# Kernel tuning notes

Measured on AMD Instinct MI355X. Metric: run time of the kernel, lower is better.

## Reference

```python
import jax, jax.numpy as jnp
import numpy as np

B, N, S = 4, 16384, 16384
C1, C2 = 256, 256
D_MODEL, NHEAD, OUT_DIM = 256, 8, 256
HEAD_DIM = D_MODEL // NHEAD
EPS_ATTN = 1e-6


def _layernorm(x, g, b, eps=1e-5):
    mu = jnp.mean(x, axis=-1, keepdims=True)
    var = jnp.mean(jnp.square(x - mu), axis=-1, keepdims=True)
    return (x - mu) * jax.lax.rsqrt(var + eps) * g + b


def setup_inputs() -> dict:
    key = jax.random.key(0)
    ks = jax.random.split(key, 20)
    def w(k, shape, fan_in):
        return jax.random.normal(k, shape, jnp.float32) * (1.0 / np.sqrt(fan_in))
    return {
        "feat1": jax.random.normal(ks[0], (B, C1, N), jnp.float32),
        "xyz1": jax.random.normal(ks[1], (B, N, 3), jnp.float32),
        "feat2": jax.random.normal(ks[2], (B, C2, S), jnp.float32),
        "xyz2": jax.random.normal(ks[3], (B, S, 3), jnp.float32),
        # pos_mlp2: Linear(3, d_model) -> ReLU -> Linear(d_model, feat2_dim)
        "pos_w1": w(ks[4], (D_MODEL, 3), 3),
        "pos_b1": jnp.zeros((D_MODEL,), jnp.float32),
        "pos_w2": w(ks[5], (C2, D_MODEL), D_MODEL),
        "pos_b2": jnp.zeros((C2,), jnp.float32),
        "q_w": w(ks[6], (D_MODEL, C1), C1),
        "k_w": w(ks[7], (D_MODEL, C2), C2),
        "v_w": w(ks[8], (D_MODEL, C2), C2),
        "merge_w": w(ks[9], (D_MODEL, D_MODEL), D_MODEL),
        # mlp: Linear(C1 + d_model, 2*d_model) -> ReLU -> Linear(2*d_model, out_dim)
        "mlp_w1": w(ks[10], (2 * D_MODEL, C1 + D_MODEL), C1 + D_MODEL),
        "mlp_w2": w(ks[11], (OUT_DIM, 2 * D_MODEL), 2 * D_MODEL),
        "ln1_g": jnp.ones((D_MODEL,), jnp.float32),
        "ln1_b": jnp.zeros((D_MODEL,), jnp.float32),
        "ln2_g": jnp.ones((OUT_DIM,), jnp.float32),
        "ln2_b": jnp.zeros((OUT_DIM,), jnp.float32),
    }


def reference(feat1, xyz1, feat2, xyz2, pos_w1, pos_b1, pos_w2, pos_b2,
              q_w, k_w, v_w, merge_w, mlp_w1, mlp_w2,
              ln1_g, ln1_b, ln2_g, ln2_b):
    bs = feat1.shape[0]
    f1 = jnp.transpose(feat1, (0, 2, 1))  # [B, N, C1]
    f2 = jnp.transpose(feat2, (0, 2, 1))  # [B, S, C2]
    # positional MLP on xyz2 added to feat2
    pos = jax.nn.relu(xyz2 @ pos_w1.T + pos_b1) @ pos_w2.T + pos_b2
    f2p = f2 + pos
    q = (f1 @ q_w.T).reshape(bs, -1, NHEAD, HEAD_DIM)   # [B, N, H, D]
    k = (f2 @ k_w.T).reshape(bs, -1, NHEAD, HEAD_DIM)   # [B, S, H, D]
    v = (f2p @ v_w.T).reshape(bs, -1, NHEAD, HEAD_DIM)  # [B, S, H, D]
    # Linear attention (elu feature map)
    Q = jax.nn.elu(q) + 1.0
    K = jax.nn.elu(k) + 1.0
    v_len = v.shape[1]
    V = v / v_len
    KV = jnp.einsum('nshd,nshv->nhdv', K, V)                 # [B, H, D, D]
    Z = 1.0 / (jnp.einsum('nlhd,nhd->nlh', Q, K.sum(axis=1)) + EPS_ATTN)
    msg = jnp.einsum('nlhd,nhdv,nlh->nlhv', Q, KV, Z) * v_len  # [B, N, H, D]
    msg = msg.reshape(bs, -1, NHEAD * HEAD_DIM) @ merge_w.T
    msg = _layernorm(msg, ln1_g, ln1_b)
    msg = jnp.concatenate([f1, msg], axis=2)
    msg = jax.nn.relu(msg @ mlp_w1.T) @ mlp_w2.T
    msg = _layernorm(msg, ln2_g, ln2_b)
    return jnp.transpose(msg, (0, 2, 1))  # [B, out_dim, N]
```

## Files before the change

### kernel.cpp

```cpp
#include <hip/hip_runtime.h>


typedef float f32x4 __attribute__((ext_vector_type(4)));
typedef __bf16 bf16x8 __attribute__((ext_vector_type(8)));
typedef __bf16 bf16x4 __attribute__((ext_vector_type(4)));

#define MFMA16(a, b, c) __builtin_amdgcn_mfma_f32_16x16x32_bf16((a), (b), (c), 0, 0, 0)

__device__ __forceinline__ void gll16(const __bf16* g, __bf16* l) {
    __builtin_amdgcn_global_load_lds(
        (const __attribute__((address_space(1))) void*)g,
        (__attribute__((address_space(3))) void*)l, 16, 0, 0);
}

__global__ __launch_bounds__(256) void prep_weights_kernel(
    const float* __restrict__ s0, const float* __restrict__ s1,
    const float* __restrict__ s2, const float* __restrict__ s3,
    const float* __restrict__ s4, const float* __restrict__ s5,
    const float* __restrict__ s6,
    __bf16* __restrict__ d0, __bf16* __restrict__ d1, __bf16* __restrict__ d2,
    __bf16* __restrict__ d3, __bf16* __restrict__ d4, __bf16* __restrict__ d5,
    __bf16* __restrict__ d6, float* __restrict__ zbase)
{
    int idx = blockIdx.x * 256 + threadIdx.x;
    if (idx < 327680) {
        int seg = idx >> 16, off = idx & 65535;
        const float* s = (seg == 0) ? s0 : (seg == 1) ? s1 : (seg == 2) ? s2 : (seg == 3) ? s3 : s4;
        __bf16* d = (seg == 0) ? d0 : (seg == 1) ? d1 : (seg == 2) ? d2 : (seg == 3) ? d3 : d4;
        d[off] = (__bf16)s[off];
    } else if (idx < 589824) {
        int off = idx - 327680; d5[off] = (__bf16)s5[off];
    } else if (idx < 720896) {
        int off = idx - 589824; d6[off] = (__bf16)s6[off];
    } else if (idx < 754688) {
        zbase[idx - 720896] = 0.f;
    }
}

__global__ __launch_bounds__(256) void pos_hidden_kernel(
    const float* __restrict__ xyz2, const float* __restrict__ pw1,
    const float* __restrict__ pb1, __bf16* __restrict__ Hid)
{
    const int tid = threadIdx.x;
    size_t tok = (size_t)blockIdx.x * 8 + (tid >> 5);
    int c0 = (tid & 31) * 8;
    const float* xz = xyz2 + tok * 3;
    float x = xz[0], y = xz[1], z = xz[2];
    bf16x8 o;
    #pragma unroll
    for (int j = 0; j < 8; ++j) {
        const float* wr = pw1 + (size_t)(c0 + j) * 3;
        float h = fmaf(x, wr[0], fmaf(y, wr[1], fmaf(z, wr[2], pb1[c0 + j])));
        o[j] = (__bf16)fmaxf(h, 0.f);
    }
    *(bf16x8*)(Hid + tok * 256 + c0) = o;
}

__global__ __launch_bounds__(256) void transpose_cast_kernel(
    const float* __restrict__ In, __bf16* __restrict__ Outb)
{
    const int tid = threadIdx.x;
    const int t0 = blockIdx.x * 64, c0 = blockIdx.y * 64;
    const size_t b = blockIdx.z;
    __shared__ __bf16 tile[64 * 72];
    #pragma unroll
    for (int i = 0; i < 4; ++i) {
        int c = i * 16 + (tid >> 4);
        int t4 = (tid & 15) * 4;
        float4 v = *(const float4*)(In + (b * 256 + c0 + c) * 16384 + t0 + t4);
        tile[(t4 + 0) * 72 + c] = (__bf16)v.x;
        tile[(t4 + 1) * 72 + c] = (__bf16)v.y;
        tile[(t4 + 2) * 72 + c] = (__bf16)v.z;
        tile[(t4 + 3) * 72 + c] = (__bf16)v.w;
    }
    __syncthreads();
    #pragma unroll
    for (int i = 0; i < 2; ++i) {
        int chunk = tid + i * 256;
        int tr = chunk >> 3, c8 = (chunk & 7) * 8;
        bf16x8 v = *(const bf16x8*)(tile + tr * 72 + c8);
        *(bf16x8*)(Outb + (b * 16384 + t0 + tr) * 256 + c0 + c8) = v;
    }
}

enum { EPI_STORE = 0, EPI_ELU = 1, EPI_ADDB = 2, EPI_RELU = 3, EPI_ELU_KSUM = 4 };

template <int EPI, bool SPLIT>
__global__ __launch_bounds__(256, 4) void gemm_tok(
    const __bf16* __restrict__ Wg,
    const __bf16* __restrict__ A0,
    const __bf16* __restrict__ A1,
    __bf16* __restrict__ Outg,
    const float* __restrict__ bias,
    const __bf16* __restrict__ addg,
    float* __restrict__ KSg,
    int K, int Cout)
{
    const int tid = threadIdx.x, w = tid >> 6, l = tid & 63, lm = l & 15;
    const int gm0 = blockIdx.x * 128, gn0 = blockIdx.y * 128;
    const size_t b = blockIdx.z;
    const __bf16* A0b = A0 + b * 16384 * (size_t)256;
    const __bf16* A1b = SPLIT ? (A1 + b * 16384 * (size_t)256) : nullptr;
    __bf16* Outb = Outg + b * 16384 * (size_t)Cout;
    const __bf16* addb = (EPI == EPI_ADDB) ? (addg + b * 16384 * (size_t)256) : nullptr;

    __shared__ __bf16 Alds[2][128 * 32];
    __shared__ __bf16 Wlds[2][128 * 32];
    __shared__ float kred[16 * 64];

    f32x4 acc[4][4];
    #pragma unroll
    for (int i = 0; i < 4; ++i)
        #pragma unroll
        for (int j = 0; j < 4; ++j) acc[i][j] = (f32x4){0.f, 0.f, 0.f, 0.f};

    const int wm = (w >> 1) * 64, wn = (w & 1) * 64;
    const int srow = tid >> 2, scol = (tid & 3) * 8;
    const int koff = (l >> 4) * 8;
    const int wbase = w * 512;

    auto stage = [&](int buf, int ks) {
        const __bf16* As = A0b; int kk = ks;
        if (SPLIT && ks >= 256) { As = A1b; kk = ks - 256; }
        gll16(As + (size_t)(gm0 + srow) * 256 + kk + scol,      &Alds[buf][wbase]);
        gll16(As + (size_t)(gm0 + 64 + srow) * 256 + kk + scol, &Alds[buf][2048 + wbase]);
        gll16(Wg + (size_t)(gn0 + srow) * K + ks + scol,        &Wlds[buf][wbase]);
        gll16(Wg + (size_t)(gn0 + 64 + srow) * K + ks + scol,   &Wlds[buf][2048 + wbase]);
    };

    stage(0, 0);
    __syncthreads();
    int cur = 0;
    for (int ks = 0; ks < K; ks += 32) {
        if (ks + 32 < K) stage(cur ^ 1, ks + 32);
        bf16x8 af[4], wf[4];
        #pragma unroll
        for (int mf = 0; mf < 4; ++mf)
            af[mf] = *(const bf16x8*)&Alds[cur][(wm + mf * 16 + lm) * 32 + koff];
        #pragma unroll
        for (int nf = 0; nf < 4; ++nf)
            wf[nf] = *(const bf16x8*)&Wlds[cur][(wn + nf * 16 + lm) * 32 + koff];
        #pragma unroll
        for (int mf = 0; mf < 4; ++mf)
            #pragma unroll
            for (int nf = 0; nf < 4; ++nf)
                acc[mf][nf] = MFMA16(af[mf], wf[nf], acc[mf][nf]);
        __syncthreads();
        cur ^= 1;
    }

    const int r0 = (l >> 4) * 4;
    float kpart[4] = {0.f, 0.f, 0.f, 0.f};
    #pragma unroll
    for (int mf = 0; mf < 4; ++mf) {
        #pragma unroll
        for (int nf = 0; nf < 4; ++nf) {
            int tok = gm0 + wm + mf * 16 + r0;
            int ch  = gn0 + wn + nf * 16 + lm;
            #pragma unroll
            for (int r = 0; r < 4; ++r) {
                float v = acc[mf][nf][r];
                if (EPI == EPI_ELU || EPI == EPI_ELU_KSUM)
                    v = (v > 0.f) ? (v + 1.f) : __expf(v);
                if (EPI == EPI_RELU) v = fmaxf(v, 0.f);
                if (EPI == EPI_ADDB) v = v + bias[ch] + (float)addb[(size_t)(tok + r) * 256 + ch];
                if (EPI == EPI_ELU_KSUM) kpart[nf] += v;
                Outb[(size_t)(tok + r) * Cout + ch] = (__bf16)v;
            }
        }
    }
    if (EPI == EPI_ELU_KSUM) {
        #pragma unroll
        for (int nf = 0; nf < 4; ++nf)
            kred[(w * 4 + (l >> 4)) * 64 + nf * 16 + lm] = kpart[nf];
        __syncthreads();
        if (tid < 128) {
            int c = tid;
            int wsel = (c >= 64) ? 1 : 0;
            float s = 0.f;
            #pragma unroll
            for (int q = 0; q < 4; ++q)
                s += kred[((wsel * 4) + q) * 64 + (c & 63)]
                   + kred[(((wsel + 2) * 4) + q) * 64 + (c & 63)];
            atomicAdd(&KSg[b * 256 + gn0 + c], s);
        }
    }
}

__global__ __launch_bounds__(256) void kv_kernel(
    const __bf16* __restrict__ Kb, const __bf16* __restrict__ Vb,
    float* __restrict__ KVg)
{
    const int tid = threadIdx.x, w = tid >> 6, l = tid & 63, lm = l & 15;
    const int sc = blockIdx.x, h = blockIdx.y, b = blockIdx.z;
    __shared__ __bf16 kT[32 * 264];
    __shared__ __bf16 vT[32 * 264];
    __shared__ float red[4 * 32 * 32];

    f32x4 acc[2][2];
    #pragma unroll
    for (int i = 0; i < 2; ++i)
        #pragma unroll
        for (int j = 0; j < 2; ++j) acc[i][j] = (f32x4){0.f, 0.f, 0.f, 0.f};

    const int koff = (l >> 4) * 8, r0 = (l >> 4) * 4;
    const size_t rowbase = (size_t)b * 16384;
    bf16x4 kreg[8], vreg[8];
    auto loadsub = [&](int sub) {
        int s0 = sc * 1024 + sub * 256;
        #pragma unroll
        for (int pass = 0; pass < 8; ++pass) {
            int sl = pass * 32 + (tid >> 3);
            int c4 = (tid & 7) * 4;
            kreg[pass] = *(const bf16x4*)(Kb + (rowbase + s0 + sl) * 256 + h * 32 + c4);
            vreg[pass] = *(const bf16x4*)(Vb + (rowbase + s0 + sl) * 256 + h * 32 + c4);
        }
    };
    loadsub(0);
    for (int sub = 0; sub < 4; ++sub) {
        __syncthreads();
        #pragma unroll
        for (int pass = 0; pass < 8; ++pass) {
            int sl = pass * 32 + (tid >> 3);
            int c4 = (tid & 7) * 4;
            #pragma unroll
            for (int i = 0; i < 4; ++i) {
                kT[(c4 + i) * 264 + sl] = kreg[pass][i];
                vT[(c4 + i) * 264 + sl] = vreg[pass][i];
            }
        }
        __syncthreads();
        if (sub < 3) loadsub(sub + 1);
        #pragma unroll
        for (int kq = 0; kq < 2; ++kq) {
            int sb = w * 64 + kq * 32;
            bf16x8 af[2], bfr[2];
            #pragma unroll
            for (int mf = 0; mf < 2; ++mf)
                af[mf] = *(const bf16x8*)(kT + (mf * 16 + lm) * 264 + sb + koff);
            #pragma unroll
            for (int nf = 0; nf < 2; ++nf)
                bfr[nf] = *(const bf16x8*)(vT + (nf * 16 + lm) * 264 + sb + koff);
            #pragma unroll
            for (int mf = 0; mf < 2; ++mf)
                #pragma unroll
                for (int nf = 0; nf < 2; ++nf)
                    acc[mf][nf] = MFMA16(af[mf], bfr[nf], acc[mf][nf]);
        }
    }
    #pragma unroll
    for (int mf = 0; mf < 2; ++mf)
        #pragma unroll
        for (int nf = 0; nf < 2; ++nf)
            #pragma unroll
            for (int r = 0; r < 4; ++r) {
                int d = mf * 16 + r0 + r, e = nf * 16 + lm;
                red[w * 1024 + d * 32 + e] = acc[mf][nf][r];
            }
    __syncthreads();
    #pragma unroll
    for (int i = 0; i < 4; ++i) {
        int idx = tid + i * 256;
        float s = red[idx] + red[1024 + idx] + red[2048 + idx] + red[3072 + idx];
        atomicAdd(&KVg[((size_t)(b * 8 + h)) * 1024 + idx], s);
    }
}

__global__ __launch_bounds__(256) void attn_apply(
    const __bf16* __restrict__ Qb, const float* __restrict__ KVg,
    const float* __restrict__ KSg, __bf16* __restrict__ Msg)
{
    const int tid = threadIdx.x, w = tid >> 6, l = tid & 63, lm = l & 15;
    const int tok0 = blockIdx.x * 64;
    const size_t b = blockIdx.y;
    __shared__ __bf16 kvT[8 * 32 * 40];
    __shared__ float ks_lds[256], z_lds[64 * 8];

    const float* KVb = KVg + b * 8192;
    #pragma unroll
    for (int i = 0; i < 32; ++i) {
        int idx = tid + i * 256;
        int h = idx >> 10, d = (idx >> 5) & 31, e = idx & 31;
        kvT[(h * 32 + e) * 40 + d] = (__bf16)KVb[idx];
    }
    ks_lds[tid] = KSg[b * 256 + tid];
    __syncthreads();

    const __bf16* Qbase = Qb + (b * 16384 + tok0) * (size_t)256;
    #pragma unroll
    for (int i = 0; i < 2; ++i) {
        int p = tid + i * 256;
        int tok = p >> 3, h = p & 7;
        const __bf16* qr = Qbase + (size_t)tok * 256 + h * 32;
        float s = 0.f;
        #pragma unroll
        for (int j = 0; j < 4; ++j) {
            bf16x8 q8 = *(const bf16x8*)(qr + j * 8);
            #pragma unroll
            for (int t = 0; t < 8; ++t) s += (float)q8[t] * ks_lds[h * 32 + j * 8 + t];
        }
        z_lds[tok * 8 + h] = 1.f / (s + 1e-6f);
    }
    __syncthreads();

    const int koff = (l >> 4) * 8, r0 = (l >> 4) * 4;
    const f32x4 zero4 = (f32x4){0.f, 0.f, 0.f, 0.f};
    #pragma unroll
    for (int h = 0; h < 8; ++h) {
        bf16x8 af = *(const bf16x8*)(Qbase + (size_t)(w * 16 + lm) * 256 + h * 32 + koff);
        #pragma unroll
        for (int nf = 0; nf < 2; ++nf) {
            bf16x8 bv = *(const bf16x8*)(kvT + (h * 32 + nf * 16 + lm) * 40 + koff);
            f32x4 m = MFMA16(af, bv, zero4);
            #pragma unroll
            for (int r = 0; r < 4; ++r) {
                int tok = w * 16 + r0 + r;
                Msg[(b * 16384 + tok0 + tok) * (size_t)256 + h * 32 + nf * 16 + lm] =
                    (__bf16)(m[r] * z_lds[tok * 8 + h]);
            }
        }
    }
}

template <bool TRANS>
__global__ __launch_bounds__(256, 2) void gemm_ln(
    const __bf16* __restrict__ Ag,
    const __bf16* __restrict__ Wg,
    const float* __restrict__ gv, const float* __restrict__ bv,
    __bf16* __restrict__ OutB,
    float* __restrict__ OutF,
    int K)
{
    const int tid = threadIdx.x, w = tid >> 6, l = tid & 63, lm = l & 15;
    const int tok0 = blockIdx.x * 128;
    const size_t b = blockIdx.y;
    const size_t trow = b * 16384 + tok0;

    __shared__ __align__(16) char smem[49152];
    __bf16* AldsB = (__bf16*)smem;
    __bf16* WldsB = (__bf16*)(smem + 16384);
    __shared__ float red1[512], red2[512], mu_lds[128], rs_lds[128];
    __shared__ float g_lds[256], b_lds[256];
    g_lds[tid] = gv[tid];
    b_lds[tid] = bv[tid];

    f32x4 acc[8][4];
    #pragma unroll
    for (int i = 0; i < 8; ++i)
        #pragma unroll
        for (int j = 0; j < 4; ++j) acc[i][j] = (f32x4){0.f, 0.f, 0.f, 0.f};

    const int srow = tid >> 2, scol = (tid & 3) * 8;
    const int koff = (l >> 4) * 8, wn = w * 64, wbase = w * 512;

    auto stage = [&](int buf, int ks) {
        gll16(Ag + (trow + srow) * K + ks + scol,      AldsB + buf * 4096 + wbase);
        gll16(Ag + (trow + 64 + srow) * K + ks + scol, AldsB + buf * 4096 + 2048 + wbase);
        #pragma unroll
        for (int c = 0; c < 4; ++c)
            gll16(Wg + (size_t)(c * 64 + srow) * K + ks + scol,
                  WldsB + buf * 8192 + c * 2048 + wbase);
    };

    stage(0, 0);
    __syncthreads();
    int cur = 0;
    for (int ks = 0; ks < K; ks += 32) {
        if (ks + 32 < K) stage(cur ^ 1, ks + 32);
        bf16x8 af[8], wf[4];
        #pragma unroll
        for (int mf = 0; mf < 8; ++mf)
            af[mf] = *(const bf16x8*)(AldsB + cur * 4096 + (mf * 16 + lm) * 32 + koff);
        #pragma unroll
        for (int nf = 0; nf < 4; ++nf)
            wf[nf] = *(const bf16x8*)(WldsB + cur * 8192 + (wn + nf * 16 + lm) * 32 + koff);
        #pragma unroll
        for (int mf = 0; mf < 8; ++mf)
            #pragma unroll
            for (int nf = 0; nf < 4; ++nf)
                acc[mf][nf] = MFMA16(af[mf], wf[nf], acc[mf][nf]);
        __syncthreads();
        cur ^= 1;
    }

    const int r0 = (l >> 4) * 4;
    #pragma unroll
    for (int mf = 0; mf < 8; ++mf) {
        #pragma unroll
        for (int r = 0; r < 4; ++r) {
            float s1 = 0.f, s2 = 0.f;
            #pragma unroll
            for (int nf = 0; nf < 4; ++nf) { float v = acc[mf][nf][r]; s1 += v; s2 += v * v; }
            #pragma unroll
            for (int m = 1; m < 16; m <<= 1) { s1 += __shfl_xor(s1, m, 64); s2 += __shfl_xor(s2, m, 64); }
            if (lm == 0) {
                red1[w * 128 + mf * 16 + r0 + r] = s1;
                red2[w * 128 + mf * 16 + r0 + r] = s2;
            }
        }
    }
    __syncthreads();
    if (tid < 128) {
        float s1 = red1[tid] + red1[128 + tid] + red1[256 + tid] + red1[384 + tid];
        float s2 = red2[tid] + red2[128 + tid] + red2[256 + tid] + red2[384 + tid];
        float mu = s1 * (1.f / 256.f);
        mu_lds[tid] = mu;
        rs_lds[tid] = rsqrtf(s2 * (1.f / 256.f) - mu * mu + 1e-5f);
    }
    __syncthreads();

    if (TRANS) {
        float* wb = (float*)smem + w * 2112;
        #pragma unroll
        for (int nf = 0; nf < 4; ++nf) {
            __syncthreads();
            float gg = g_lds[wn + nf * 16 + lm], bb = b_lds[wn + nf * 16 + lm];
            #pragma unroll
            for (int mf = 0; mf < 8; ++mf) {
                int tl = mf * 16 + r0;
                f32x4 v;
                #pragma unroll
                for (int r = 0; r < 4; ++r)
                    v[r] = (acc[mf][nf][r] - mu_lds[tl + r]) * rs_lds[tl + r] * gg + bb;
                *(f32x4*)(wb + lm * 132 + tl) = v;
            }
            __syncthreads();
            #pragma unroll
            for (int t = 0; t < 8; ++t) {
                int row = t * 2 + (l >> 5);
                int col = (l & 31) * 4;
                f32x4 v = *(const f32x4*)(wb + row * 132 + col);
                *(f32x4*)(OutF + (b * 256 + wn + nf * 16 + row) * (size_t)16384 + tok0 + col) = v;
            }
        }
    } else {
        #pragma unroll
        for (int mf = 0; mf < 8; ++mf) {
            #pragma unroll
            for (int nf = 0; nf < 4; ++nf) {
                int ch = wn + nf * 16 + lm;
                #pragma unroll
                for (int r = 0; r < 4; ++r) {
                    int tl = mf * 16 + r0 + r;
                    float y = (acc[mf][nf][r] - mu_lds[tl]) * rs_lds[tl] * g_lds[ch] + b_lds[ch];
                    OutB[(trow + tl) * (size_t)256 + ch] = (__bf16)y;
                }
            }
        }
    }
}

extern "C" void kernel_launch(void* const* d_in, const int* in_sizes, int n_in,
                              void* d_out, int out_size, void* d_ws, size_t ws_size,
                              hipStream_t stream) {
    const float* feat1   = (const float*)d_in[0];
    const float* feat2   = (const float*)d_in[2];
    const float* xyz2    = (const float*)d_in[3];
    const float* pos_w1  = (const float*)d_in[4];
    const float* pos_b1  = (const float*)d_in[5];
    const float* pos_w2  = (const float*)d_in[6];
    const float* pos_b2  = (const float*)d_in[7];
    const float* q_w     = (const float*)d_in[8];
    const float* k_w     = (const float*)d_in[9];
    const float* v_w     = (const float*)d_in[10];
    const float* merge_w = (const float*)d_in[11];
    const float* mlp_w1  = (const float*)d_in[12];
    const float* mlp_w2  = (const float*)d_in[13];
    const float* ln1_g   = (const float*)d_in[14];
    const float* ln1_b   = (const float*)d_in[15];
    const float* ln2_g   = (const float*)d_in[16];
    const float* ln2_b   = (const float*)d_in[17];
    float* outp = (float*)d_out;

    char* ws = (char*)d_ws;
    size_t off = 0;
    auto alloc = [&](size_t bytes) { char* p = ws + off; off += (bytes + 255) & ~(size_t)255; return p; };
    const size_t ACT = (size_t)4 * 16384 * 256 * 2;
    __bf16* WQ  = (__bf16*)alloc(65536 * 2);
    __bf16* WK  = (__bf16*)alloc(65536 * 2);
    __bf16* WV  = (__bf16*)alloc(65536 * 2);
    __bf16* WM  = (__bf16*)alloc(65536 * 2);
    __bf16* WP2 = (__bf16*)alloc(65536 * 2);
    __bf16* W1  = (__bf16*)alloc(262144 * 2);
    __bf16* W2  = (__bf16*)alloc(131072 * 2);
    float*  KV  = (float*)alloc(4 * 8 * 32 * 32 * 4);
    float*  KS  = (float*)alloc(4 * 256 * 4);
    __bf16* F1T = (__bf16*)alloc(ACT);
    __bf16* HID = (__bf16*)alloc(ACT);
    __bf16* F2T = (__bf16*)alloc(ACT);
    __bf16* F2P = (__bf16*)alloc(ACT);
    __bf16* KB  = (__bf16*)alloc(ACT);
    __bf16* VB  = (__bf16*)alloc(ACT);
    __bf16* QB  = (__bf16*)alloc(ACT);
    __bf16* H1     = HID;
    __bf16* MSGRAW = F2T;
    __bf16* MSG1   = F2P;
    if (ws_size < off) return;

    prep_weights_kernel<<<2948, 256, 0, stream>>>(q_w, k_w, v_w, merge_w, pos_w2,
                                                  mlp_w1, mlp_w2,
                                                  WQ, WK, WV, WM, WP2, W1, W2, KV);
    pos_hidden_kernel<<<8192, 256, 0, stream>>>(xyz2, pos_w1, pos_b1, HID);
    transpose_cast_kernel<<<dim3(256, 4, 4), 256, 0, stream>>>(feat1, F1T);
    transpose_cast_kernel<<<dim3(256, 4, 4), 256, 0, stream>>>(feat2, F2T);
    gemm_tok<EPI_ADDB, false><<<dim3(128, 2, 4), 256, 0, stream>>>(WP2, HID, nullptr, F2P, pos_b2, F2T, nullptr, 256, 256);
    gemm_tok<EPI_ELU_KSUM, false><<<dim3(128, 2, 4), 256, 0, stream>>>(WK, F2T, nullptr, KB, nullptr, nullptr, KS, 256, 256);
    gemm_tok<EPI_STORE, false><<<dim3(128, 2, 4), 256, 0, stream>>>(WV, F2P, nullptr, VB, nullptr, nullptr, nullptr, 256, 256);
    gemm_tok<EPI_ELU, false><<<dim3(128, 2, 4), 256, 0, stream>>>(WQ, F1T, nullptr, QB, nullptr, nullptr, nullptr, 256, 256);
    kv_kernel<<<dim3(16, 8, 4), 256, 0, stream>>>(KB, VB, KV);
    attn_apply<<<dim3(256, 4), 256, 0, stream>>>(QB, KV, KS, MSGRAW);
    gemm_ln<false><<<dim3(128, 4), 256, 0, stream>>>(MSGRAW, WM, ln1_g, ln1_b, MSG1, nullptr, 256);
    gemm_tok<EPI_RELU, true><<<dim3(128, 4, 4), 256, 0, stream>>>(W1, F1T, MSG1, H1, nullptr, nullptr, nullptr, 512, 512);
    gemm_ln<true><<<dim3(128, 4), 256, 0, stream>>>(H1, W2, ln2_g, ln2_b, nullptr, outp, 512);
    (void)in_sizes; (void)n_in; (void)out_size;
}
```

Baseline: 454.2 us.

## Fuse pos-MLP+V, Q+attention+merge+LN, and MLP+LN into chained-GEMM kernels

Replaces the chain of separate token GEMMs with three fused kernels. One computes the positional hidden layer on the fly and feeds it into the V projection. One does the Q projection, ELU, normalizer, KV apply, merge GEMM and LayerNorm. One runs both MLP GEMMs plus the final LayerNorm with a transposed store. Intermediates stay in swizzled LDS tiles instead of round-tripping through HBM, which removes several full-activation reads and writes and kernel launches. The cost is large LDS use with one 512-thread block per CU, and grids of only 512–1024 blocks, so occupancy and latency hiding drop.

```diff
diff --git a/kernel.cpp b/kernel.cpp
--- a/kernel.cpp
+++ b/kernel.cpp
@@ -37,25 +37,6 @@
     }
 }
 
-__global__ __launch_bounds__(256) void pos_hidden_kernel(
-    const float* __restrict__ xyz2, const float* __restrict__ pw1,
-    const float* __restrict__ pb1, __bf16* __restrict__ Hid)
-{
-    const int tid = threadIdx.x;
-    size_t tok = (size_t)blockIdx.x * 8 + (tid >> 5);
-    int c0 = (tid & 31) * 8;
-    const float* xz = xyz2 + tok * 3;
-    float x = xz[0], y = xz[1], z = xz[2];
-    bf16x8 o;
-    #pragma unroll
-    for (int j = 0; j < 8; ++j) {
-        const float* wr = pw1 + (size_t)(c0 + j) * 3;
-        float h = fmaf(x, wr[0], fmaf(y, wr[1], fmaf(z, wr[2], pb1[c0 + j])));
-        o[j] = (__bf16)fmaxf(h, 0.f);
-    }
-    *(bf16x8*)(Hid + tok * 256 + c0) = o;
-}
-
 __global__ __launch_bounds__(256) void transpose_cast_kernel(
     const float* __restrict__ In, __bf16* __restrict__ Outb)
 {
@@ -83,26 +64,15 @@
     }
 }
 
-enum { EPI_STORE = 0, EPI_ELU = 1, EPI_ADDB = 2, EPI_RELU = 3, EPI_ELU_KSUM = 4 };
-
-template <int EPI, bool SPLIT>
-__global__ __launch_bounds__(256, 4) void gemm_tok(
-    const __bf16* __restrict__ Wg,
-    const __bf16* __restrict__ A0,
-    const __bf16* __restrict__ A1,
-    __bf16* __restrict__ Outg,
-    const float* __restrict__ bias,
-    const __bf16* __restrict__ addg,
-    float* __restrict__ KSg,
-    int K, int Cout)
+__global__ __launch_bounds__(256, 4) void kgemm_kernel(
+    const __bf16* __restrict__ Wg, const __bf16* __restrict__ A0,
+    __bf16* __restrict__ Outg, float* __restrict__ KSg)
 {
     const int tid = threadIdx.x, w = tid >> 6, l = tid & 63, lm = l & 15;
     const int gm0 = blockIdx.x * 128, gn0 = blockIdx.y * 128;
     const size_t b = blockIdx.z;
     const __bf16* A0b = A0 + b * 16384 * (size_t)256;
-    const __bf16* A1b = SPLIT ? (A1 + b * 16384 * (size_t)256) : nullptr;
-    __bf16* Outb = Outg + b * 16384 * (size_t)Cout;
-    const __bf16* addb = (EPI == EPI_ADDB) ? (addg + b * 16384 * (size_t)256) : nullptr;
+    __bf16* Outb = Outg + b * 16384 * (size_t)256;
 
     __shared__ __bf16 Alds[2][128 * 32];
     __shared__ __bf16 Wlds[2][128 * 32];
@@ -120,19 +90,16 @@
     const int wbase = w * 512;
 
     auto stage = [&](int buf, int ks) {
-        const __bf16* As = A0b; int kk = ks;
-        if (SPLIT && ks >= 256) { As = A1b; kk = ks - 256; }
-        gll16(As + (size_t)(gm0 + srow) * 256 + kk + scol,      &Alds[buf][wbase]);
-        gll16(As + (size_t)(gm0 + 64 + srow) * 256 + kk + scol, &Alds[buf][2048 + wbase]);
-        gll16(Wg + (size_t)(gn0 + srow) * K + ks + scol,        &Wlds[buf][wbase]);
-        gll16(Wg + (size_t)(gn0 + 64 + srow) * K + ks + scol,   &Wlds[buf][2048 + wbase]);
+        gll16(A0b + (size_t)(gm0 + srow) * 256 + ks + scol,      &Alds[buf][wbase]);
+        gll16(A0b + (size_t)(gm0 + 64 + srow) * 256 + ks + scol, &Alds[buf][2048 + wbase]);
+        gll16(Wg + (size_t)(gn0 + srow) * 256 + ks + scol,       &Wlds[buf][wbase]);
+        gll16(Wg + (size_t)(gn0 + 64 + srow) * 256 + ks + scol,  &Wlds[buf][2048 + wbase]);
     };
-
     stage(0, 0);
     __syncthreads();
     int cur = 0;
-    for (int ks = 0; ks < K; ks += 32) {
-        if (ks + 32 < K) stage(cur ^ 1, ks + 32);
+    for (int ks = 0; ks < 256; ks += 32) {
+        if (ks + 32 < 256) stage(cur ^ 1, ks + 32);
         bf16x8 af[4], wf[4];
         #pragma unroll
         for (int mf = 0; mf < 4; ++mf)
@@ -160,31 +127,159 @@
             #pragma unroll
             for (int r = 0; r < 4; ++r) {
                 float v = acc[mf][nf][r];
-                if (EPI == EPI_ELU || EPI == EPI_ELU_KSUM)
-                    v = (v > 0.f) ? (v + 1.f) : __expf(v);
-                if (EPI == EPI_RELU) v = fmaxf(v, 0.f);
-                if (EPI == EPI_ADDB) v = v + bias[ch] + (float)addb[(size_t)(tok + r) * 256 + ch];
-                if (EPI == EPI_ELU_KSUM) kpart[nf] += v;
-                Outb[(size_t)(tok + r) * Cout + ch] = (__bf16)v;
-            }
-        }
-    }
-    if (EPI == EPI_ELU_KSUM) {
+                v = (v > 0.f) ? (v + 1.f) : __expf(v);
+                kpart[nf] += v;
+                Outb[(size_t)(tok + r) * 256 + ch] = (__bf16)v;
+            }
+        }
+    }
+    #pragma unroll
+    for (int nf = 0; nf < 4; ++nf)
+        kred[(w * 4 + (l >> 4)) * 64 + nf * 16 + lm] = kpart[nf];
+    __syncthreads();
+    if (tid < 128) {
+        int c = tid;
+        int wsel = (c >= 64) ? 1 : 0;
+        float s = 0.f;
+        #pragma unroll
+        for (int q = 0; q < 4; ++q)
+            s += kred[((wsel * 4) + q) * 64 + (c & 63)]
+               + kred[(((wsel + 2) * 4) + q) * 64 + (c & 63)];
+        atomicAdd(&KSg[b * 256 + gn0 + c], s);
+    }
+}
+
+__global__ __launch_bounds__(512, 1) void fuse_pv(
+    const float* __restrict__ xyz2, const float* __restrict__ pw1g,
+    const float* __restrict__ pb1g, const __bf16* __restrict__ WP2,
+    const float* __restrict__ pb2g, const __bf16* __restrict__ F2Tg,
+    const __bf16* __restrict__ WVg, __bf16* __restrict__ VBg)
+{
+    const int tid = threadIdx.x, w = tid >> 6, l = tid & 63, lm = l & 15;
+    const int tok0 = blockIdx.x * 128;
+    const size_t b = blockIdx.y;
+    const int wtm = w >> 2, wtn = w & 3;
+    const int koff = (l >> 4) * 8, r0 = (l >> 4) * 4;
+
+    __shared__ __bf16 tile[128 * 256];
+    __shared__ __bf16 wstage[2][256 * 32];
+    __shared__ float pw1[256 * 4];
+    __shared__ float pb1[256], pb2[256];
+
+    if (tid < 256) {
+        pw1[tid * 4 + 0] = pw1g[tid * 3 + 0];
+        pw1[tid * 4 + 1] = pw1g[tid * 3 + 1];
+        pw1[tid * 4 + 2] = pw1g[tid * 3 + 2];
+        pb1[tid] = pb1g[tid];
+        pb2[tid] = pb2g[tid];
+    }
+    const __bf16* F2Tb = F2Tg + ((size_t)b * 16384 + tok0) * 256;
+    #pragma unroll
+    for (int i = 0; i < 8; ++i) {
+        int row = i * 16 + w * 2 + (l >> 5);
+        int col = ((l & 31) * 8) ^ ((row & 7) * 8);
+        gll16(F2Tb + (size_t)row * 256 + col, tile + i * 4096 + w * 512 + (l & 31) * 8);
+    }
+    float xr[4], yr[4], zr[4];
+    #pragma unroll
+    for (int mf = 0; mf < 4; ++mf) {
+        size_t tg = (size_t)b * 16384 + tok0 + wtm * 64 + mf * 16 + lm;
+        xr[mf] = xyz2[tg * 3 + 0]; yr[mf] = xyz2[tg * 3 + 1]; zr[mf] = xyz2[tg * 3 + 2];
+    }
+
+    auto stageW = [&](int buf, const __bf16* Wsrc, int ks) {
+        #pragma unroll
+        for (int j = 0; j < 2; ++j)
+            gll16(Wsrc + (size_t)(j * 128 + (tid >> 2)) * 256 + ks + (tid & 3) * 8,
+                  &wstage[buf][j * 4096 + tid * 8]);
+    };
+
+    f32x4 acc[4][4];
+    #pragma unroll
+    for (int i = 0; i < 4; ++i)
+        #pragma unroll
+        for (int j = 0; j < 4; ++j) acc[i][j] = (f32x4){0.f, 0.f, 0.f, 0.f};
+    stageW(0, WP2, 0);
+    __syncthreads();
+    int cur = 0;
+    for (int ks = 0; ks < 256; ks += 32) {
+        if (ks + 32 < 256) stageW(cur ^ 1, WP2, ks + 32);
+        bf16x8 af[4];
+        #pragma unroll
+        for (int mf = 0; mf < 4; ++mf)
+            #pragma unroll
+            for (int j = 0; j < 8; ++j) {
+                int k = ks + koff + j;
+                float h = fmaf(xr[mf], pw1[k * 4],
+                          fmaf(yr[mf], pw1[k * 4 + 1],
+                          fmaf(zr[mf], pw1[k * 4 + 2], pb1[k])));
+                af[mf][j] = (__bf16)fmaxf(h, 0.f);
+            }
+        bf16x8 wf[4];
         #pragma unroll
         for (int nf = 0; nf < 4; ++nf)
-            kred[(w * 4 + (l >> 4)) * 64 + nf * 16 + lm] = kpart[nf];
-        __syncthreads();
-        if (tid < 128) {
-            int c = tid;
-            int wsel = (c >= 64) ? 1 : 0;
-            float s = 0.f;
-            #pragma unroll
-            for (int q = 0; q < 4; ++q)
-                s += kred[((wsel * 4) + q) * 64 + (c & 63)]
-                   + kred[(((wsel + 2) * 4) + q) * 64 + (c & 63)];
-            atomicAdd(&KSg[b * 256 + gn0 + c], s);
-        }
-    }
+            wf[nf] = *(const bf16x8*)&wstage[cur][(wtn * 64 + nf * 16 + lm) * 32 + koff];
+        #pragma unroll
+        for (int mf = 0; mf < 4; ++mf)
+            #pragma unroll
+            for (int nf = 0; nf < 4; ++nf)
+                acc[mf][nf] = MFMA16(af[mf], wf[nf], acc[mf][nf]);
+        __syncthreads();
+        cur ^= 1;
+    }
+    stageW(0, WVg, 0);
+    #pragma unroll
+    for (int mf = 0; mf < 4; ++mf)
+        #pragma unroll
+        for (int nf = 0; nf < 4; ++nf) {
+            int ch = wtn * 64 + nf * 16 + lm;
+            #pragma unroll
+            for (int r = 0; r < 4; ++r) {
+                int tl = wtm * 64 + mf * 16 + r0 + r;
+                int addr = tl * 256 + (ch ^ ((tl & 7) * 8));
+                float v = acc[mf][nf][r] + pb2[ch] + (float)tile[addr];
+                tile[addr] = (__bf16)v;
+            }
+        }
+    __syncthreads();
+
+    f32x4 acc2[4][4];
+    #pragma unroll
+    for (int i = 0; i < 4; ++i)
+        #pragma unroll
+        for (int j = 0; j < 4; ++j) acc2[i][j] = (f32x4){0.f, 0.f, 0.f, 0.f};
+    cur = 0;
+    for (int ks = 0; ks < 256; ks += 32) {
+        if (ks + 32 < 256) stageW(cur ^ 1, WVg, ks + 32);
+        bf16x8 af[4], wf[4];
+        #pragma unroll
+        for (int mf = 0; mf < 4; ++mf) {
+            int row = wtm * 64 + mf * 16 + lm;
+            af[mf] = *(const bf16x8*)&tile[row * 256 + ((ks + koff) ^ ((lm & 7) * 8))];
+        }
+        #pragma unroll
+        for (int nf = 0; nf < 4; ++nf)
+            wf[nf] = *(const bf16x8*)&wstage[cur][(wtn * 64 + nf * 16 + lm) * 32 + koff];
+        #pragma unroll
+        for (int mf = 0; mf < 4; ++mf)
+            #pragma unroll
+            for (int nf = 0; nf < 4; ++nf)
+                acc2[mf][nf] = MFMA16(af[mf], wf[nf], acc2[mf][nf]);
+        __syncthreads();
+        cur ^= 1;
+    }
+    __bf16* VBb = VBg + ((size_t)b * 16384 + tok0) * 256;
+    #pragma unroll
+    for (int mf = 0; mf < 4; ++mf)
+        #pragma unroll
+        for (int nf = 0; nf < 4; ++nf) {
+            int ch = wtn * 64 + nf * 16 + lm;
+            #pragma unroll
+            for (int r = 0; r < 4; ++r) {
+                int tl = wtm * 64 + mf * 16 + r0 + r;
+                VBb[(size_t)tl * 256 + ch] = (__bf16)acc2[mf][nf][r];
+            }
+        }
 }
 
 __global__ __launch_bounds__(256) void kv_kernel(
@@ -266,187 +361,371 @@
     }
 }
 
-__global__ __launch_bounds__(256) void attn_apply(
-    const __bf16* __restrict__ Qb, const float* __restrict__ KVg,
-    const float* __restrict__ KSg, __bf16* __restrict__ Msg)
+__global__ __launch_bounds__(512, 1) void qattn(
+    const __bf16* __restrict__ F1Tg, const __bf16* __restrict__ WQg,
+    const float* __restrict__ KVg, const float* __restrict__ KSg,
+    const __bf16* __restrict__ WMg, const float* __restrict__ g1,
+    const float* __restrict__ b1, __bf16* __restrict__ MSG1g)
+{
+    const int tid = threadIdx.x, w = tid >> 6, l = tid & 63, lm = l & 15;
+    const int tok0 = blockIdx.x * 128;
+    const size_t b = blockIdx.y;
+    const int wtm = w >> 2, wtn = w & 3;
+    const int koff = (l >> 4) * 8, r0 = (l >> 4) * 4;
+
+    __shared__ __bf16 qtile[128 * 256];
+    __shared__ __bf16 astage[2][128 * 32];
+    __shared__ __bf16 wstage[2][256 * 32];
+    __shared__ __bf16 kvT[8 * 32 * 40];
+    __shared__ float ks_lds[256], z_lds[128 * 8];
+    __shared__ float red1[4][128], red2[4][128], mu_lds[128], rs_lds[128];
+    __shared__ float g_lds[256], b_lds[256];
+
+    if (tid < 256) {
+        ks_lds[tid] = KSg[b * 256 + tid];
+        g_lds[tid] = g1[tid];
+        b_lds[tid] = b1[tid];
+    }
+    const float* KVb = KVg + b * 8192;
+    #pragma unroll
+    for (int i = 0; i < 16; ++i) {
+        int idx = tid + i * 512;
+        int h = idx >> 10, d = (idx >> 5) & 31, e = idx & 31;
+        kvT[(h * 32 + e) * 40 + d] = (__bf16)KVb[idx];
+    }
+
+    const __bf16* F1Tb = F1Tg + ((size_t)b * 16384 + tok0) * 256;
+    auto stageA = [&](int buf, int ks) {
+        gll16(F1Tb + (size_t)(tid >> 2) * 256 + ks + (tid & 3) * 8, &astage[buf][tid * 8]);
+    };
+    auto stageW = [&](int buf, const __bf16* Wsrc, int ks) {
+        #pragma unroll
+        for (int j = 0; j < 2; ++j)
+            gll16(Wsrc + (size_t)(j * 128 + (tid >> 2)) * 256 + ks + (tid & 3) * 8,
+                  &wstage[buf][j * 4096 + tid * 8]);
+    };
+
+    f32x4 acc[4][4];
+    #pragma unroll
+    for (int i = 0; i < 4; ++i)
+        #pragma unroll
+        for (int j = 0; j < 4; ++j) acc[i][j] = (f32x4){0.f, 0.f, 0.f, 0.f};
+    stageA(0, 0); stageW(0, WQg, 0);
+    __syncthreads();
+    int cur = 0;
+    for (int ks = 0; ks < 256; ks += 32) {
+        if (ks + 32 < 256) { stageA(cur ^ 1, ks + 32); stageW(cur ^ 1, WQg, ks + 32); }
+        bf16x8 af[4], wf[4];
+        #pragma unroll
+        for (int mf = 0; mf < 4; ++mf)
+            af[mf] = *(const bf16x8*)&astage[cur][(wtm * 64 + mf * 16 + lm) * 32 + koff];
+        #pragma unroll
+        for (int nf = 0; nf < 4; ++nf)
+            wf[nf] = *(const bf16x8*)&wstage[cur][(wtn * 64 + nf * 16 + lm) * 32 + koff];
+        #pragma unroll
+        for (int mf = 0; mf < 4; ++mf)
+            #pragma unroll
+            for (int nf = 0; nf < 4; ++nf)
+                acc[mf][nf] = MFMA16(af[mf], wf[nf], acc[mf][nf]);
+        __syncthreads();
+        cur ^= 1;
+    }
+    stageW(0, WMg, 0);
+    #pragma unroll
+    for (int mf = 0; mf < 4; ++mf)
+        #pragma unroll
+        for (int nf = 0; nf < 4; ++nf) {
+            int ch = wtn * 64 + nf * 16 + lm;
+            #pragma unroll
+            for (int r = 0; r < 4; ++r) {
+                int tl = wtm * 64 + mf * 16 + r0 + r;
+                float v = acc[mf][nf][r];
+                v = (v > 0.f) ? (v + 1.f) : __expf(v);
+                qtile[tl * 256 + (ch ^ ((tl & 7) * 8))] = (__bf16)v;
+            }
+        }
+    __syncthreads();
+
+    #pragma unroll
+    for (int i = 0; i < 2; ++i) {
+        int p = tid + i * 512;
+        int tok = p >> 3, h = p & 7;
+        float s = 0.f;
+        #pragma unroll
+        for (int d = 0; d < 32; ++d)
+            s += (float)qtile[tok * 256 + ((h * 32 + d) ^ ((tok & 7) * 8))] * ks_lds[h * 32 + d];
+        z_lds[tok * 8 + h] = 1.f / (s + 1e-6f);
+    }
+    __syncthreads();
+
+    f32x4 macc[4][4];
+    const f32x4 zero4 = (f32x4){0.f, 0.f, 0.f, 0.f};
+    #pragma unroll
+    for (int hh = 0; hh < 2; ++hh) {
+        int h = wtn * 2 + hh;
+        bf16x8 af[4], wf[2];
+        #pragma unroll
+        for (int mf = 0; mf < 4; ++mf) {
+            int row = wtm * 64 + mf * 16 + lm;
+            af[mf] = *(const bf16x8*)&qtile[row * 256 + ((h * 32 + koff) ^ ((lm & 7) * 8))];
+        }
+        #pragma unroll
+        for (int nf = 0; nf < 2; ++nf)
+            wf[nf] = *(const bf16x8*)&kvT[(h * 32 + nf * 16 + lm) * 40 + koff];
+        #pragma unroll
+        for (int mf = 0; mf < 4; ++mf)
+            #pragma unroll
+            for (int nf = 0; nf < 2; ++nf)
+                macc[mf][hh * 2 + nf] = MFMA16(af[mf], wf[nf], zero4);
+    }
+    __syncthreads();
+    #pragma unroll
+    for (int mf = 0; mf < 4; ++mf)
+        #pragma unroll
+        for (int hh = 0; hh < 2; ++hh)
+            #pragma unroll
+            for (int nf = 0; nf < 2; ++nf) {
+                int h = wtn * 2 + hh;
+                int ch = wtn * 64 + hh * 32 + nf * 16 + lm;
+                #pragma unroll
+                for (int r = 0; r < 4; ++r) {
+                    int tl = wtm * 64 + mf * 16 + r0 + r;
+                    float v = macc[mf][hh * 2 + nf][r] * z_lds[tl * 8 + h];
+                    qtile[tl * 256 + (ch ^ ((tl & 7) * 8))] = (__bf16)v;
+                }
+            }
+    __syncthreads();
+
+    f32x4 acc3[4][4];
+    #pragma unroll
+    for (int i = 0; i < 4; ++i)
+        #pragma unroll
+        for (int j = 0; j < 4; ++j) acc3[i][j] = (f32x4){0.f, 0.f, 0.f, 0.f};
+    cur = 0;
+    for (int ks = 0; ks < 256; ks += 32) {
+        if (ks + 32 < 256) stageW(cur ^ 1, WMg, ks + 32);
+        bf16x8 af[4], wf[4];
+        #pragma unroll
+        for (int mf = 0; mf < 4; ++mf) {
+            int row = wtm * 64 + mf * 16 + lm;
+            af[mf] = *(const bf16x8*)&qtile[row * 256 + ((ks + koff) ^ ((lm & 7) * 8))];
+        }
+        #pragma unroll
+        for (int nf = 0; nf < 4; ++nf)
+            wf[nf] = *(const bf16x8*)&wstage[cur][(wtn * 64 + nf * 16 + lm) * 32 + koff];
+        #pragma unroll
+        for (int mf = 0; mf < 4; ++mf)
+            #pragma unroll
+            for (int nf = 0; nf < 4; ++nf)
+                acc3[mf][nf] = MFMA16(af[mf], wf[nf], acc3[mf][nf]);
+        __syncthreads();
+        cur ^= 1;
+    }
+    #pragma unroll
+    for (int mf = 0; mf < 4; ++mf)
+        #pragma unroll
+        for (int r = 0; r < 4; ++r) {
+            float s1 = 0.f, s2 = 0.f;
+            #pragma unroll
+            for (int nf = 0; nf < 4; ++nf) { float v = acc3[mf][nf][r]; s1 += v; s2 += v * v; }
+            #pragma unroll
+            for (int m = 1; m < 16; m <<= 1) { s1 += __shfl_xor(s1, m, 64); s2 += __shfl_xor(s2, m, 64); }
+            if (lm == 0) {
+                int row = wtm * 64 + mf * 16 + r0 + r;
+                red1[wtn][row] = s1;
+                red2[wtn][row] = s2;
+            }
+        }
+    __syncthreads();
+    if (tid < 128) {
+        float s1 = red1[0][tid] + red1[1][tid] + red1[2][tid] + red1[3][tid];
+        float s2 = red2[0][tid] + red2[1][tid] + red2[2][tid] + red2[3][tid];
+        float mu = s1 * (1.f / 256.f);
+        mu_lds[tid] = mu;
+        rs_lds[tid] = rsqrtf(s2 * (1.f / 256.f) - mu * mu + 1e-5f);
+    }
+    __syncthreads();
+    __bf16* Mb = MSG1g + ((size_t)b * 16384 + tok0) * 256;
+    #pragma unroll
+    for (int mf = 0; mf < 4; ++mf)
+        #pragma unroll
+        for (int nf = 0; nf < 4; ++nf) {
+            int ch = wtn * 64 + nf * 16 + lm;
+            #pragma unroll
+            for (int r = 0; r < 4; ++r) {
+                int tl = wtm * 64 + mf * 16 + r0 + r;
+                float y = (acc3[mf][nf][r] - mu_lds[tl]) * rs_lds[tl] * g_lds[ch] + b_lds[ch];
+                Mb[(size_t)tl * 256 + ch] = (__bf16)y;
+            }
+        }
+}
+
+__global__ __launch_bounds__(512, 1) void mlp_fused(
+    const __bf16* __restrict__ F1Tg, const __bf16* __restrict__ MSG1g,
+    const __bf16* __restrict__ W1g, const __bf16* __restrict__ W2g,
+    const float* __restrict__ g2, const float* __restrict__ b2,
+    float* __restrict__ Outg)
 {
     const int tid = threadIdx.x, w = tid >> 6, l = tid & 63, lm = l & 15;
     const int tok0 = blockIdx.x * 64;
     const size_t b = blockIdx.y;
-    __shared__ __bf16 kvT[8 * 32 * 40];
-    __shared__ float ks_lds[256], z_lds[64 * 8];
-
-    const float* KVb = KVg + b * 8192;
-    #pragma unroll
-    for (int i = 0; i < 32; ++i) {
-        int idx = tid + i * 256;
-        int h = idx >> 10, d = (idx >> 5) & 31, e = idx & 31;
-        kvT[(h * 32 + e) * 40 + d] = (__bf16)KVb[idx];
-    }
-    ks_lds[tid] = KSg[b * 256 + tid];
-    __syncthreads();
-
-    const __bf16* Qbase = Qb + (b * 16384 + tok0) * (size_t)256;
-    #pragma unroll
-    for (int i = 0; i < 2; ++i) {
-        int p = tid + i * 256;
-        int tok = p >> 3, h = p & 7;
-        const __bf16* qr = Qbase + (size_t)tok * 256 + h * 32;
-        float s = 0.f;
-        #pragma unroll
-        for (int j = 0; j < 4; ++j) {
-            bf16x8 q8 = *(const bf16x8*)(qr + j * 8);
-            #pragma unroll
-            for (int t = 0; t < 8; ++t) s += (float)q8[t] * ks_lds[h * 32 + j * 8 + t];
-        }
-        z_lds[tok * 8 + h] = 1.f / (s + 1e-6f);
-    }
-    __syncthreads();
-
+    const int wtm = w >> 2, wtn = w & 3;
     const int koff = (l >> 4) * 8, r0 = (l >> 4) * 4;
-    const f32x4 zero4 = (f32x4){0.f, 0.f, 0.f, 0.f};
-    #pragma unroll
-    for (int h = 0; h < 8; ++h) {
-        bf16x8 af = *(const bf16x8*)(Qbase + (size_t)(w * 16 + lm) * 256 + h * 32 + koff);
-        #pragma unroll
-        for (int nf = 0; nf < 2; ++nf) {
-            bf16x8 bv = *(const bf16x8*)(kvT + (h * 32 + nf * 16 + lm) * 40 + koff);
-            f32x4 m = MFMA16(af, bv, zero4);
+
+    __shared__ __bf16 h1[64 * 512];
+    __shared__ __bf16 astage[2][64 * 32];
+    __shared__ __align__(16) char wsmem[65536];
+    __bf16* wstage0 = (__bf16*)wsmem;
+    __bf16* wstage1 = (__bf16*)(wsmem + 32768);
+    __shared__ float red1[4][64], red2[4][64], mu_lds[64], rs_lds[64];
+    __shared__ float g_lds[256], b_lds[256];
+
+    if (tid < 256) { g_lds[tid] = g2[tid]; b_lds[tid] = b2[tid]; }
+
+    const __bf16* F1Tb  = F1Tg  + ((size_t)b * 16384 + tok0) * 256;
+    const __bf16* MSG1b = MSG1g + ((size_t)b * 16384 + tok0) * 256;
+
+    auto stageA = [&](int buf, int ks) {
+        if (tid < 256) {
+            const __bf16* src = (ks < 256) ? F1Tb : MSG1b;
+            int kk = ks & 255;
+            gll16(src + (size_t)(tid >> 2) * 256 + kk + (tid & 3) * 8, &astage[buf][tid * 8]);
+        }
+    };
+    auto stageW1 = [&](int buf, int ks) {
+        __bf16* dst = buf ? wstage1 : wstage0;
+        #pragma unroll
+        for (int i = 0; i < 4; ++i)
+            gll16(W1g + (size_t)(i * 128 + (tid >> 2)) * 512 + ks + (tid & 3) * 8,
+                  dst + i * 4096 + tid * 8);
+    };
+    auto stageW2 = [&](int buf, int ks) {
+        __bf16* dst = buf ? wstage1 : wstage0;
+        #pragma unroll
+        for (int i = 0; i < 2; ++i)
+            gll16(W2g + (size_t)(i * 128 + (tid >> 2)) * 512 + ks + (tid & 3) * 8,
+                  dst + i * 4096 + tid * 8);
+    };
+
+    f32x4 acc[2][8];
+    #pragma unroll
+    for (int i = 0; i < 2; ++i)
+        #pragma unroll
+        for (int j = 0; j < 8; ++j) acc[i][j] = (f32x4){0.f, 0.f, 0.f, 0.f};
+    stageA(0, 0); stageW1(0, 0);
+    __syncthreads();
+    int cur = 0;
+    for (int ks = 0; ks < 512; ks += 32) {
+        if (ks + 32 < 512) { stageA(cur ^ 1, ks + 32); stageW1(cur ^ 1, ks + 32); }
+        __bf16* wst = cur ? wstage1 : wstage0;
+        bf16x8 af[2], wf[8];
+        #pragma unroll
+        for (int mf = 0; mf < 2; ++mf)
+            af[mf] = *(const bf16x8*)&astage[cur][(wtm * 32 + mf * 16 + lm) * 32 + koff];
+        #pragma unroll
+        for (int nf = 0; nf < 8; ++nf)
+            wf[nf] = *(const bf16x8*)(wst + (wtn * 128 + nf * 16 + lm) * 32 + koff);
+        #pragma unroll
+        for (int mf = 0; mf < 2; ++mf)
+            #pragma unroll
+            for (int nf = 0; nf < 8; ++nf)
+                acc[mf][nf] = MFMA16(af[mf], wf[nf], acc[mf][nf]);
+        __syncthreads();
+        cur ^= 1;
+    }
+    stageW2(0, 0);
+    #pragma unroll
+    for (int mf = 0; mf < 2; ++mf)
+        #pragma unroll
+        for (int nf = 0; nf < 8; ++nf) {
+            int ch = wtn * 128 + nf * 16 + lm;
             #pragma unroll
             for (int r = 0; r < 4; ++r) {
-                int tok = w * 16 + r0 + r;
-                Msg[(b * 16384 + tok0 + tok) * (size_t)256 + h * 32 + nf * 16 + lm] =
-                    (__bf16)(m[r] * z_lds[tok * 8 + h]);
-            }
-        }
-    }
-}
-
-template <bool TRANS>
-__global__ __launch_bounds__(256, 2) void gemm_ln(
-    const __bf16* __restrict__ Ag,
-    const __bf16* __restrict__ Wg,
-    const float* __restrict__ gv, const float* __restrict__ bv,
-    __bf16* __restrict__ OutB,
-    float* __restrict__ OutF,
-    int K)
-{
-    const int tid = threadIdx.x, w = tid >> 6, l = tid & 63, lm = l & 15;
-    const int tok0 = blockIdx.x * 128;
-    const size_t b = blockIdx.y;
-    const size_t trow = b * 16384 + tok0;
-
-    __shared__ __align__(16) char smem[49152];
-    __bf16* AldsB = (__bf16*)smem;
-    __bf16* WldsB = (__bf16*)(smem + 16384);
-    __shared__ float red1[512], red2[512], mu_lds[128], rs_lds[128];
-    __shared__ float g_lds[256], b_lds[256];
-    g_lds[tid] = gv[tid];
-    b_lds[tid] = bv[tid];
-
-    f32x4 acc[8][4];
-    #pragma unroll
-    for (int i = 0; i < 8; ++i)
-        #pragma unroll
-        for (int j = 0; j < 4; ++j) acc[i][j] = (f32x4){0.f, 0.f, 0.f, 0.f};
-
-    const int srow = tid >> 2, scol = (tid & 3) * 8;
-    const int koff = (l >> 4) * 8, wn = w * 64, wbase = w * 512;
-
-    auto stage = [&](int buf, int ks) {
-        gll16(Ag + (trow + srow) * K + ks + scol,      AldsB + buf * 4096 + wbase);
-        gll16(Ag + (trow + 64 + srow) * K + ks + scol, AldsB + buf * 4096 + 2048 + wbase);
-        #pragma unroll
-        for (int c = 0; c < 4; ++c)
-            gll16(Wg + (size_t)(c * 64 + srow) * K + ks + scol,
-                  WldsB + buf * 8192 + c * 2048 + wbase);
-    };
-
-    stage(0, 0);
-    __syncthreads();
-    int cur = 0;
-    for (int ks = 0; ks < K; ks += 32) {
-        if (ks + 32 < K) stage(cur ^ 1, ks + 32);
-        bf16x8 af[8], wf[4];
-        #pragma unroll
-        for (int mf = 0; mf < 8; ++mf)
-            af[mf] = *(const bf16x8*)(AldsB + cur * 4096 + (mf * 16 + lm) * 32 + koff);
+                int tl = wtm * 32 + mf * 16 + r0 + r;
+                float v = fmaxf(acc[mf][nf][r], 0.f);
+                h1[tl * 512 + (ch ^ ((tl & 7) * 8))] = (__bf16)v;
+            }
+        }
+    __syncthreads();
+
+    f32x4 acc2[2][4];
+    #pragma unroll
+    for (int i = 0; i < 2; ++i)
+        #pragma unroll
+        for (int j = 0; j < 4; ++j) acc2[i][j] = (f32x4){0.f, 0.f, 0.f, 0.f};
+    cur = 0;
+    for (int ks = 0; ks < 512; ks += 32) {
+        if (ks + 32 < 512) stageW2(cur ^ 1, ks + 32);
+        __bf16* wst = cur ? wstage1 : wstage0;
+        bf16x8 af[2], wf[4];
+        #pragma unroll
+        for (int mf = 0; mf < 2; ++mf) {
+            int row = wtm * 32 + mf * 16 + lm;
+            af[mf] = *(const bf16x8*)&h1[row * 512 + ((ks + koff) ^ ((lm & 7) * 8))];
+        }
         #pragma unroll
         for (int nf = 0; nf < 4; ++nf)
-            wf[nf] = *(const bf16x8*)(WldsB + cur * 8192 + (wn + nf * 16 + lm) * 32 + koff);
-        #pragma unroll
-        for (int mf = 0; mf < 8; ++mf)
+            wf[nf] = *(const bf16x8*)(wst + (wtn * 64 + nf * 16 + lm) * 32 + koff);
+        #pragma unroll
+        for (int mf = 0; mf < 2; ++mf)
             #pragma unroll
             for (int nf = 0; nf < 4; ++nf)
-                acc[mf][nf] = MFMA16(af[mf], wf[nf], acc[mf][nf]);
+                acc2[mf][nf] = MFMA16(af[mf], wf[nf], acc2[mf][nf]);
         __syncthreads();
         cur ^= 1;
     }
-
-    const int r0 = (l >> 4) * 4;
-    #pragma unroll
-    for (int mf = 0; mf < 8; ++mf) {
+    #pragma unroll
+    for (int mf = 0; mf < 2; ++mf)
         #pragma unroll
         for (int r = 0; r < 4; ++r) {
             float s1 = 0.f, s2 = 0.f;
             #pragma unroll
-            for (int nf = 0; nf < 4; ++nf) { float v = acc[mf][nf][r]; s1 += v; s2 += v * v; }
+            for (int nf = 0; nf < 4; ++nf) { float v = acc2[mf][nf][r]; s1 += v; s2 += v * v; }
             #pragma unroll
             for (int m = 1; m < 16; m <<= 1) { s1 += __shfl_xor(s1, m, 64); s2 += __shfl_xor(s2, m, 64); }
             if (lm == 0) {
-                red1[w * 128 + mf * 16 + r0 + r] = s1;
-                red2[w * 128 + mf * 16 + r0 + r] = s2;
-            }
-        }
-    }
-    __syncthreads();
-    if (tid < 128) {
-        float s1 = red1[tid] + red1[128 + tid] + red1[256 + tid] + red1[384 + tid];
-        float s2 = red2[tid] + red2[128 + tid] + red2[256 + tid] + red2[384 + tid];
+                int row = wtm * 32 + mf * 16 + r0 + r;
+                red1[wtn][row] = s1;
+                red2[wtn][row] = s2;
+            }
+        }
+    __syncthreads();
+    if (tid < 64) {
+        float s1 = red1[0][tid] + red1[1][tid] + red1[2][tid] + red1[3][tid];
+        float s2 = red2[0][tid] + red2[1][tid] + red2[2][tid] + red2[3][tid];
         float mu = s1 * (1.f / 256.f);
         mu_lds[tid] = mu;
         rs_lds[tid] = rsqrtf(s2 * (1.f / 256.f) - mu * mu + 1e-5f);
     }
     __syncthreads();
-
-    if (TRANS) {
-        float* wb = (float*)smem + w * 2112;
-        #pragma unroll
-        for (int nf = 0; nf < 4; ++nf) {
-            __syncthreads();
-            float gg = g_lds[wn + nf * 16 + lm], bb = b_lds[wn + nf * 16 + lm];
-            #pragma unroll
-            for (int mf = 0; mf < 8; ++mf) {
-                int tl = mf * 16 + r0;
-                f32x4 v;
+    float* bounce = (float*)wsmem;
+    #pragma unroll
+    for (int half = 0; half < 2; ++half) {
+        if ((wtn >> 1) == half) {
+            #pragma unroll
+            for (int mf = 0; mf < 2; ++mf)
                 #pragma unroll
-                for (int r = 0; r < 4; ++r)
-                    v[r] = (acc[mf][nf][r] - mu_lds[tl + r]) * rs_lds[tl + r] * gg + bb;
-                *(f32x4*)(wb + lm * 132 + tl) = v;
-            }
-            __syncthreads();
-            #pragma unroll
-            for (int t = 0; t < 8; ++t) {
-                int row = t * 2 + (l >> 5);
-                int col = (l & 31) * 4;
-                f32x4 v = *(const f32x4*)(wb + row * 132 + col);
-                *(f32x4*)(OutF + (b * 256 + wn + nf * 16 + row) * (size_t)16384 + tok0 + col) = v;
-            }
-        }
-    } else {
-        #pragma unroll
-        for (int mf = 0; mf < 8; ++mf) {
-            #pragma unroll
-            for (int nf = 0; nf < 4; ++nf) {
-                int ch = wn + nf * 16 + lm;
-                #pragma unroll
-                for (int r = 0; r < 4; ++r) {
-                    int tl = mf * 16 + r0 + r;
-                    float y = (acc[mf][nf][r] - mu_lds[tl]) * rs_lds[tl] * g_lds[ch] + b_lds[ch];
-                    OutB[(trow + tl) * (size_t)256 + ch] = (__bf16)y;
+                for (int nf = 0; nf < 4; ++nf) {
+                    int chl = (wtn & 1) * 64 + nf * 16 + lm;
+                    int ch  = half * 128 + chl;
+                    #pragma unroll
+                    for (int r = 0; r < 4; ++r) {
+                        int tl = wtm * 32 + mf * 16 + r0 + r;
+                        bounce[chl * 68 + tl] =
+                            (acc2[mf][nf][r] - mu_lds[tl]) * rs_lds[tl] * g_lds[ch] + b_lds[ch];
+                    }
                 }
-            }
-        }
+        }
+        __syncthreads();
+        {
+            int row = tid >> 2, seg = tid & 3;
+            float* src = bounce + row * 68 + seg * 16;
+            float* dst = Outg + ((size_t)b * 256 + half * 128 + row) * 16384 + tok0 + seg * 16;
+            #pragma unroll
+            for (int j = 0; j < 4; ++j)
+                *(f32x4*)(dst + j * 4) = *(const f32x4*)(src + j * 4);
+        }
+        __syncthreads();
     }
 }
 
@@ -486,31 +765,22 @@
     float*  KV  = (float*)alloc(4 * 8 * 32 * 32 * 4);
     float*  KS  = (float*)alloc(4 * 256 * 4);
     __bf16* F1T = (__bf16*)alloc(ACT);
-    __bf16* HID = (__bf16*)alloc(ACT);
     __bf16* F2T = (__bf16*)alloc(ACT);
-    __bf16* F2P = (__bf16*)alloc(ACT);
     __bf16* KB  = (__bf16*)alloc(ACT);
     __bf16* VB  = (__bf16*)alloc(ACT);
-    __bf16* QB  = (__bf16*)alloc(ACT);
-    __bf16* H1     = HID;
-    __bf16* MSGRAW = F2T;
-    __bf16* MSG1   = F2P;
+    __bf16* MSG1 = (__bf16*)alloc(ACT);
     if (ws_size < off) return;
 
     prep_weights_kernel<<<2948, 256, 0, stream>>>(q_w, k_w, v_w, merge_w, pos_w2,
                                                   mlp_w1, mlp_w2,
                                                   WQ, WK, WV, WM, WP2, W1, W2, KV);
-    pos_hidden_kernel<<<8192, 256, 0, stream>>>(xyz2, pos_w1, pos_b1, HID);
     transpose_cast_kernel<<<dim3(256, 4, 4), 256, 0, stream>>>(feat1, F1T);
     transpose_cast_kernel<<<dim3(256, 4, 4), 256, 0, stream>>>(feat2, F2T);
-    gemm_tok<EPI_ADDB, false><<<dim3(128, 2, 4), 256, 0, stream>>>(WP2, HID, nullptr, F2P, pos_b2, F2T, nullptr, 256, 256);
-    gemm_tok<EPI_ELU_KSUM, false><<<dim3(128, 2, 4), 256, 0, stream>>>(WK, F2T, nullptr, KB, nullptr, nullptr, KS, 256, 256);
-    gemm_tok<EPI_STORE, false><<<dim3(128, 2, 4), 256, 0, stream>>>(WV, F2P, nullptr, VB, nullptr, nullptr, nullptr, 256, 256);
-    gemm_tok<EPI_ELU, false><<<dim3(128, 2, 4), 256, 0, stream>>>(WQ, F1T, nullptr, QB, nullptr, nullptr, nullptr, 256, 256);
+    fuse_pv<<<dim3(128, 4), 512, 0, stream>>>(xyz2, pos_w1, pos_b1, WP2, pos_b2,
+                                              F2T, WV, VB);
+    kgemm_kernel<<<dim3(128, 2, 4), 256, 0, stream>>>(WK, F2T, KB, KS);
     kv_kernel<<<dim3(16, 8, 4), 256, 0, stream>>>(KB, VB, KV);
-    attn_apply<<<dim3(256, 4), 256, 0, stream>>>(QB, KV, KS, MSGRAW);
-    gemm_ln<false><<<dim3(128, 4), 256, 0, stream>>>(MSGRAW, WM, ln1_g, ln1_b, MSG1, nullptr, 256);
-    gemm_tok<EPI_RELU, true><<<dim3(128, 4, 4), 256, 0, stream>>>(W1, F1T, MSG1, H1, nullptr, nullptr, nullptr, 512, 512);
-    gemm_ln<true><<<dim3(128, 4), 256, 0, stream>>>(H1, W2, ln2_g, ln2_b, nullptr, outp, 512);
+    qattn<<<dim3(128, 4), 512, 0, stream>>>(F1T, WQ, KV, KS, WM, ln1_g, ln1_b, MSG1);
+    mlp_fused<<<dim3(256, 4), 512, 0, stream>>>(F1T, MSG1, W1, W2, ln2_g, ln2_b, outp);
     (void)in_sizes; (void)n_in; (void)out_size;
 }
```

After: 458.9 us. Within noise of the previous version (+1.0%).
